# Performance work log

Measured on AMD Instinct MI355X. Metric: run time of the kernel, lower is better.

The kernel has to match this reference:

```python
import jax, jax.numpy as jnp
import numpy as np

EPS = 1e-5
HEADS, K, U, M = 4, 16, 1, 11


def _bn(z, gamma, beta, mean, var):
    # z: [b, c, n]; BN in eval mode (running stats)
    inv = jax.lax.rsqrt(var + EPS)
    return (z - mean[None, :, None]) * (gamma * inv)[None, :, None] + beta[None, :, None]


def setup_inputs() -> dict:
    key = jax.random.key(0)
    ks = jax.random.split(key, 16)
    b, C, w, h = 8, 256, 64, 64
    vv = 256 // HEADS  # out_channels // heads = 64
    inp = {}
    inp['x'] = jax.random.normal(ks[0], (b, C, w, h), dtype=jnp.float32)
    sc = 1.0 / np.sqrt(C)
    inp['Wq'] = jax.random.normal(ks[1], (K * HEADS, C), dtype=jnp.float32) * sc
    inp['q_gamma'] = jnp.ones((K * HEADS,), jnp.float32)
    inp['q_beta'] = jnp.zeros((K * HEADS,), jnp.float32)
    inp['q_mean'] = jax.random.normal(ks[2], (K * HEADS,), dtype=jnp.float32) * 0.1
    inp['q_var'] = jax.random.uniform(ks[3], (K * HEADS,), minval=0.5, maxval=1.5, dtype=jnp.float32)
    inp['Wk'] = jax.random.normal(ks[4], (K * U, C), dtype=jnp.float32) * sc
    inp['Wv'] = jax.random.normal(ks[5], (vv * U, C), dtype=jnp.float32) * sc
    inp['v_gamma'] = jnp.ones((vv * U,), jnp.float32)
    inp['v_beta'] = jnp.zeros((vv * U,), jnp.float32)
    inp['v_mean'] = jax.random.normal(ks[6], (vv * U,), dtype=jnp.float32) * 0.1
    inp['v_var'] = jax.random.uniform(ks[7], (vv * U,), minval=0.5, maxval=1.5, dtype=jnp.float32)
    inp['embedding'] = jax.random.normal(ks[8], (K, U, 1, M, M), dtype=jnp.float32)
    return inp


def reference(x, Wq, q_gamma, q_beta, q_mean, q_var, Wk, Wv,
              v_gamma, v_beta, v_mean, v_var, embedding):
    b, C, w, h = x.shape
    n = w * h
    vv = Wv.shape[0] // U
    xf = x.reshape(b, C, n)

    # queries: 1x1 conv + BN -> [b, heads, k, n]
    q = _bn(jnp.einsum('oc,bcn->bon', Wq, xf), q_gamma, q_beta, q_mean, q_var)
    q = q.reshape(b, HEADS, K, n)

    # keys: 1x1 conv, softmax over spatial positions -> [b, k, u, n]
    keys = jnp.einsum('oc,bcn->bon', Wk, xf).reshape(b, K, U, n)
    sm = jax.nn.softmax(keys, axis=-1)

    # values: 1x1 conv + BN -> [b, vv, u, n]
    values = _bn(jnp.einsum('oc,bcn->bon', Wv, xf), v_gamma, v_beta, v_mean, v_var)
    values = values.reshape(b, vv, U, n)

    # content lambda
    lam_c = jnp.einsum('bkun,bvun->bkv', sm, values)          # [b, k, vv]
    y_c = jnp.einsum('bhkn,bkv->bhvn', q, lam_c)              # [b, h, vv, n]

    # position lambda via conv3d over (vv, w, h) with kernel (1, m, m)
    v5 = values.reshape(b, U, vv, w, h)                       # torch .view reinterpret
    pad = (M - 1) // 2
    lam_p = jax.lax.conv_general_dilated(
        v5, embedding, window_strides=(1, 1, 1),
        padding=((0, 0), (pad, pad), (pad, pad)),
        dimension_numbers=('NCDHW', 'OIDHW', 'NCDHW'))        # [b, k, vv, w, h]
    lam_p = lam_p.reshape(b, K, vv, n)
    y_p = jnp.einsum('bhkn,bkvn->bhvn', q, lam_p)             # [b, h, vv, n]

    out = (y_c + y_p).reshape(b, HEADS * vv, w, h)
    return out
```

## Files before the change

kernel.cpp:

```cpp
#include <hip/hip_runtime.h>
#include <math.h>

#define EPSBN 1e-5f

constexpr int B_ = 8, C_ = 256, N_ = 4096, IMG_ = 64;
constexpr int HEADS_ = 4, K_ = 16, VV_ = 64, M_ = 11, OC_ = 144;

typedef _Float16 half4 __attribute__((ext_vector_type(4)));
typedef _Float16 half8 __attribute__((ext_vector_type(8)));
typedef __fp16 fp16x2 __attribute__((ext_vector_type(2)));
typedef float f32x4 __attribute__((ext_vector_type(4)));

constexpr size_t O_WT   = 0;
constexpr size_t O_BIAS = 18432;
constexpr size_t O_EMBT = 18688;
constexpr size_t O_Q    = 24832;
constexpr size_t O_KEYS = O_Q    + 1048576;
constexpr size_t O_SINV = O_KEYS + 524288;
constexpr size_t O_VP   = 1597952;
constexpr size_t O_LCP  = O_VP   + 1802240;
constexpr size_t O_LC   = O_LCP  + 262144;

constexpr int VPROW = 88, VPPLANE = 80 * 88;

__global__ void k_prep(const float* __restrict__ Wq,
                       const float* __restrict__ qg, const float* __restrict__ qb,
                       const float* __restrict__ qm, const float* __restrict__ qv,
                       const float* __restrict__ Wk, const float* __restrict__ Wv,
                       const float* __restrict__ vg, const float* __restrict__ vb,
                       const float* __restrict__ vm, const float* __restrict__ vva,
                       const float* __restrict__ emb, float* __restrict__ ws) {
    int t = threadIdx.x, blk = blockIdx.x;
    if (blk >= 16) {
        size_t i = (size_t)(blk - 16) * 256 + t;
        f32x4 z = {0.f, 0.f, 0.f, 0.f};
        *(f32x4*)(ws + O_VP + i * 4) = z;
        return;
    }
    _Float16* wf = (_Float16*)(ws + O_WT);
    int base = blk * 2304;
#pragma unroll
    for (int i = 0; i < 9; i++) {
        int idx = base + i * 256 + t;
        int o = idx >> 8, c = idx & 255;
        float w;
        if (o < 64) {
            float s = qg[o] * rsqrtf(qv[o] + EPSBN);
            w = Wq[o * 256 + c] * s;
        } else if (o < 80) {
            w = Wk[(o - 64) * 256 + c];
        } else {
            int ov = o - 80;
            float s = vg[ov] * rsqrtf(vva[ov] + EPSBN);
            w = Wv[ov * 256 + c] * s;
        }
        wf[idx] = (_Float16)w;
    }
    if (blk == 0 && t < 144) {
        float bias;
        if (t < 64) {
            float s = qg[t] * rsqrtf(qv[t] + EPSBN);
            bias = qb[t] - qm[t] * s;
        } else if (t < 80) {
            bias = 0.f;
        } else {
            int ov = t - 80;
            float s = vg[ov] * rsqrtf(vva[ov] + EPSBN);
            bias = vb[ov] - vm[ov] * s;
        }
        ws[O_BIAS + t] = bias;
    }
    if (blk == 15) {
        _Float16* ef = (_Float16*)(ws + O_EMBT);
        for (int idx = t; idx < 64 * 48; idx += 256) {
            int l = idx / 48, rem = idx % 48;
            int dp = rem >> 3, j = rem & 7;
            int k = l & 15, g = l >> 4;
            int dy = 2 * dp + (j >> 2);
            int dx = 4 * g + (j & 3);
            float v = (dy < 11 && dx < 11) ? emb[k * 121 + dy * 11 + dx] : 0.f;
            ef[idx] = (_Float16)v;
        }
    }
}

__global__ __launch_bounds__(256) void k_proj(const float* __restrict__ x,
                                              const float* __restrict__ wsc,
                                              float* __restrict__ ws) {
    __shared__ uint WL[144 * 68];
    __shared__ uint XL[64 * 68];
    int b    = blockIdx.y;
    int pos0 = blockIdx.x * 64;
    int t    = threadIdx.x;
    int w = t >> 6, l = t & 63;
    int g = l >> 4, r = l & 15;

    f32x4 acc[9];
#pragma unroll
    for (int mf = 0; mf < 9; mf++) acc[mf] = (f32x4){0.f, 0.f, 0.f, 0.f};

    const uint* wsrc = (const uint*)(wsc + O_WT);
    const float* xb = x + (size_t)b * C_ * N_ + pos0;
    union u4h { uint4 u; half8 h; };

    for (int kh = 0; kh < 2; kh++) {
        if (kh) __syncthreads();
#pragma unroll
        for (int i = 0; i < 9; i++) {
            int idx = t + i * 256;
            int o = idx >> 4, c4 = idx & 15;
            uint4 wv = *(const uint4*)(wsrc + o * 128 + kh * 64 + c4 * 4);
            *(uint4*)&WL[o * 68 + c4 * 4] = wv;
        }
#pragma unroll
        for (int i = 0; i < 4; i++) {
            int idx = t + i * 256;
            int cl = idx >> 4, p4 = idx & 15;
            float4 a0 = *(const float4*)(xb + (size_t)(2 * (64 * kh + cl)) * N_ + 4 * p4);
            float4 a1 = *(const float4*)(xb + (size_t)(2 * (64 * kh + cl) + 1) * N_ + 4 * p4);
            union { _Float16 h[2]; uint u; } pk;
#pragma unroll
            for (int j = 0; j < 4; j++) {
                float v0 = (j == 0) ? a0.x : (j == 1) ? a0.y : (j == 2) ? a0.z : a0.w;
                float v1 = (j == 0) ? a1.x : (j == 1) ? a1.y : (j == 2) ? a1.z : a1.w;
                pk.h[0] = (_Float16)v0; pk.h[1] = (_Float16)v1;
                XL[(4 * p4 + j) * 68 + cl] = pk.u;
            }
        }
        __syncthreads();

#pragma unroll
        for (int ks = 0; ks < 4; ks++) {
            int cu = 16 * ks + 4 * g;
            u4h bf;
            bf.u = *(const uint4*)&XL[(w * 16 + r) * 68 + cu];
#pragma unroll
            for (int mf = 0; mf < 9; mf++) {
                u4h af;
                af.u = *(const uint4*)&WL[(16 * mf + r) * 68 + cu];
                acc[mf] = __builtin_amdgcn_mfma_f32_16x16x32_f16(af.h, bf.h, acc[mf], 0, 0, 0);
            }
        }
    }

    int pos = pos0 + w * 16 + r;
#pragma unroll
    for (int mf = 0; mf < 9; mf++) {
        float4 bias4 = *(const float4*)(wsc + O_BIAS + 16 * mf + 4 * g);
        f32x4 a = acc[mf];
        float rv0 = a[0] + bias4.x, rv1 = a[1] + bias4.y;
        float rv2 = a[2] + bias4.z, rv3 = a[3] + bias4.w;
        if (mf < 4) {
            union { fp16x2 h[2]; uint2 u; } pk;
            pk.h[0] = __builtin_amdgcn_cvt_pkrtz(rv0, rv1);
            pk.h[1] = __builtin_amdgcn_cvt_pkrtz(rv2, rv3);
            ((uint2*)(ws + O_Q))[((size_t)(b * 16 + 4 * mf + g)) * N_ + pos] = pk.u;
        } else if (mf == 4) {
            int ch0 = 16 * mf + 4 * g;
            float* kp = ws + O_KEYS + ((size_t)(b * 16 + (ch0 - 64))) * N_ + pos;
            kp[0] = rv0; kp[(size_t)N_] = rv1; kp[2 * (size_t)N_] = rv2; kp[3 * (size_t)N_] = rv3;
        } else {
            int ov = 16 * mf + 4 * g - 80;
            int y = pos >> 6, xx = pos & 63;
            _Float16* vp = (_Float16*)(ws + O_VP) +
                           ((size_t)(b * 64 + ov)) * VPPLANE + (size_t)(y + 8) * VPROW + (xx + 8);
            vp[0] = (_Float16)rv0; vp[VPPLANE] = (_Float16)rv1;
            vp[2 * VPPLANE] = (_Float16)rv2; vp[3 * VPPLANE] = (_Float16)rv3;
        }
    }
}

__global__ __launch_bounds__(256) void k_ssum(float* __restrict__ ws) {
    int row = blockIdx.x;
    const float* src = ws + O_KEYS + (size_t)row * N_;
    int t = threadIdx.x;
    float s = 0.f;
#pragma unroll
    for (int i = 0; i < 4; i++) {
        float4 r = *(const float4*)(src + i * 1024 + t * 4);
        s += expf(r.x) + expf(r.y) + expf(r.z) + expf(r.w);
    }
    for (int off = 32; off > 0; off >>= 1) s += __shfl_xor(s, off);
    __shared__ float reds[4];
    if ((t & 63) == 0) reds[t >> 6] = s;
    __syncthreads();
    if (t == 0)
        ws[O_SINV + row] = 1.f / (reds[0] + reds[1] + reds[2] + reds[3]);
}

__global__ __launch_bounds__(256) void k_lamc(float* __restrict__ ws) {
    int b  = blockIdx.x >> 5;
    int ch = blockIdx.x & 31;
    int n0 = ch * 128;
    int y0r = n0 >> 6;
    __shared__ float ek[16 * 128];
    int t = threadIdx.x;
#pragma unroll
    for (int i = 0; i < 2; i++) {
        int f4 = t + i * 256;
        int k = f4 >> 5, nq = f4 & 31;
        float4 kv = *(const float4*)(ws + O_KEYS + ((size_t)(b * 16 + k)) * N_ + n0 + 4 * nq);
        float is = ws[O_SINV + b * 16 + k];
        float4 e;
        e.x = expf(kv.x) * is; e.y = expf(kv.y) * is;
        e.z = expf(kv.z) * is; e.w = expf(kv.w) * is;
        *(float4*)&ek[k * 128 + 4 * nq] = e;
    }
    __syncthreads();

    int v  = t & 63;
    int kg = __builtin_amdgcn_readfirstlane(t >> 6);
    float acc[4] = {0.f, 0.f, 0.f, 0.f};
    const _Float16* vp = (const _Float16*)(ws + O_VP) +
                         (size_t)(b * 64 + v) * VPPLANE + (size_t)(y0r + 8) * VPROW + 8;
#pragma unroll
    for (int r = 0; r < 2; r++) {
        union U4 { uint4 q; _Float16 h[8]; } u[8];
#pragma unroll
        for (int iu = 0; iu < 8; iu++)
            u[iu].q = *(const uint4*)(vp + (size_t)r * VPROW + 8 * iu);
#pragma unroll
        for (int xq = 0; xq < 16; xq++) {
            float4 e0 = *(const float4*)&ek[(kg * 4 + 0) * 128 + r * 64 + 4 * xq];
            float4 e1 = *(const float4*)&ek[(kg * 4 + 1) * 128 + r * 64 + 4 * xq];
            float4 e2 = *(const float4*)&ek[(kg * 4 + 2) * 128 + r * 64 + 4 * xq];
            float4 e3 = *(const float4*)&ek[(kg * 4 + 3) * 128 + r * 64 + 4 * xq];
            float v0 = (float)u[xq >> 1].h[(xq & 1) * 4 + 0];
            float v1 = (float)u[xq >> 1].h[(xq & 1) * 4 + 1];
            float v2 = (float)u[xq >> 1].h[(xq & 1) * 4 + 2];
            float v3 = (float)u[xq >> 1].h[(xq & 1) * 4 + 3];
            acc[0] += e0.x * v0 + e0.y * v1 + e0.z * v2 + e0.w * v3;
            acc[1] += e1.x * v0 + e1.y * v1 + e1.z * v2 + e1.w * v3;
            acc[2] += e2.x * v0 + e2.y * v1 + e2.z * v2 + e2.w * v3;
            acc[3] += e3.x * v0 + e3.y * v1 + e3.z * v2 + e3.w * v3;
        }
    }
#pragma unroll
    for (int j = 0; j < 4; j++)
        ws[O_LCP + ((size_t)(b * 32 + ch) * 16 + kg * 4 + j) * 64 + v] = acc[j];
}

__global__ void k_lcred(float* __restrict__ ws) {
    int b = blockIdx.x, t = threadIdx.x;
    float s = 0.f;
    for (int c = 0; c < 32; c++)
        s += ws[O_LCP + ((size_t)(b * 32 + c)) * 1024 + t];
    ws[O_LC + (size_t)b * 1024 + t] = s;
}

__global__ __launch_bounds__(256, 4) void k_out(const float* __restrict__ wsc,
                                                float* __restrict__ out) {
    __shared__ ushort vt[2][4][19][84];
    int ytile = blockIdx.x;
    int vc    = blockIdx.y;
    int b     = blockIdx.z;
    int y0 = ytile * 8, v0 = vc * 4;
    int t = threadIdx.x;
    int w = t >> 6, l = t & 63;
    int g = l >> 4, nb = l & 15;

    float4 lc4[4];
#pragma unroll
    for (int i = 0; i < 4; i++)
        lc4[i] = *(const float4*)(wsc + O_LC + ((size_t)(b * 16 + 4 * g + i)) * 64 + v0);

    union AF { uint4 u; half8 h; } af[6];
    {
        const uint4* ap = (const uint4*)((const _Float16*)(wsc + O_EMBT) + (size_t)l * 48);
#pragma unroll
        for (int dp = 0; dp < 6; dp++) af[dp].u = ap[dp];
    }

    const ushort* vpb = (const ushort*)(wsc + O_VP) + (size_t)(b * 64 + v0) * VPPLANE;
    for (int T = t; T < 1596; T += 256) {
        int v = T / 399, rem = T % 399;
        int r = rem / 21, qd = rem % 21;
        const ushort* src = vpb + (size_t)v * VPPLANE + (size_t)(y0 + 3 + r) * VPROW + 4 * qd;
        uint2 u01 = *(const uint2*)src;
        uint2 u23 = *(const uint2*)(src + 4);
        *(uint2*)&vt[0][v][r][4 * qd] = u01;
        uint lo = (u01.x >> 16) | (u01.y << 16);
        uint hi = (u01.y >> 16) | (u23.x << 16);
        *(uint2*)&vt[1][v][r][4 * qd] = make_uint2(lo, hi);
    }
    __syncthreads();

    const uint* vtu = (const uint*)&vt[0][0][0][0];
    const uint2* qfp = (const uint2*)(wsc + O_Q);

#pragma unroll
    for (int xt = 0; xt < 4; xt++) {
        int X = xt * 16 + nb;
        union QH { uint2 u; fp16x2 h[2]; } qh[2][4];
#pragma unroll
        for (int yy2 = 0; yy2 < 2; yy2++) {
            int pos = (y0 + 2 * w + yy2) * 64 + X;
#pragma unroll
            for (int j = 0; j < 4; j++)
                qh[yy2][j].u = qfp[((size_t)(b * 16 + 4 * (g ^ j) + g)) * N_ + pos];
        }
        int wcol = X + 4 * g + 3;
        int cp   = wcol & 1;
        int j0u  = (wcol - cp) >> 1;

#pragma unroll
        for (int v = 0; v < 4; v++) {
            int bwin = ((cp * 4 + v) * 19 + 2 * w) * 42 + j0u;
            uint2 win[13];
#pragma unroll
            for (int i = 0; i < 13; i++) {
                win[i].x = vtu[bwin + 42 * i];
                win[i].y = vtu[bwin + 42 * i + 1];
            }

#pragma unroll
            for (int yy2 = 0; yy2 < 2; yy2++) {
                f32x4 acc = {0.f, 0.f, 0.f, 0.f};
#pragma unroll
                for (int dp = 0; dp < 6; dp++) {
                    union { uint u[4]; half8 h; } bb;
                    bb.u[0] = win[yy2 + 2 * dp].x;
                    bb.u[1] = win[yy2 + 2 * dp].y;
                    bb.u[2] = win[yy2 + 2 * dp + 1].x;
                    bb.u[3] = win[yy2 + 2 * dp + 1].y;
                    acc = __builtin_amdgcn_mfma_f32_16x16x32_f16(af[dp].h, bb.h, acc, 0, 0, 0);
                }
                float d0 = acc[0] + lc4[0][v];
                float d1 = acc[1] + lc4[1][v];
                float d2 = acc[2] + lc4[2][v];
                float d3 = acc[3] + lc4[3][v];
                fp16x2 dlo = __builtin_amdgcn_cvt_pkrtz(d0, d1);
                fp16x2 dhi = __builtin_amdgcn_cvt_pkrtz(d2, d3);
                float ph[4];
#pragma unroll
                for (int j = 0; j < 4; j++)
                    ph[j] = __builtin_amdgcn_fdot2(qh[yy2][j].h[0], dlo,
                            __builtin_amdgcn_fdot2(qh[yy2][j].h[1], dhi, 0.f, false), false);
                float sa = ph[0] + __shfl_xor(ph[1], 16);
                float sb = ph[2] + __shfl_xor(ph[3], 16);
                float o  = sa + __shfl_xor(sb, 32);
                int pos = (y0 + 2 * w + yy2) * 64 + X;
                out[((size_t)(b * 256 + g * 64 + v0 + v)) * N_ + pos] = o;
            }
        }
    }
}

extern "C" void kernel_launch(void* const* d_in, const int* in_sizes, int n_in,
                              void* d_out, int out_size, void* d_ws, size_t ws_size,
                              hipStream_t stream) {
    const float* x   = (const float*)d_in[0];
    const float* Wq  = (const float*)d_in[1];
    const float* qg  = (const float*)d_in[2];
    const float* qb  = (const float*)d_in[3];
    const float* qm  = (const float*)d_in[4];
    const float* qv  = (const float*)d_in[5];
    const float* Wk  = (const float*)d_in[6];
    const float* Wv  = (const float*)d_in[7];
    const float* vg  = (const float*)d_in[8];
    const float* vb  = (const float*)d_in[9];
    const float* vm  = (const float*)d_in[10];
    const float* vva = (const float*)d_in[11];
    const float* emb = (const float*)d_in[12];
    float* ws  = (float*)d_ws;
    float* out = (float*)d_out;

    k_prep<<<1776, 256, 0, stream>>>(Wq, qg, qb, qm, qv, Wk, Wv, vg, vb, vm, vva, emb, ws);
    k_proj<<<dim3(64, 8), 256, 0, stream>>>(x, ws, ws);
    k_ssum<<<128, 256, 0, stream>>>(ws);
    k_lamc<<<256, 256, 0, stream>>>(ws);
    k_lcred<<<8, 1024, 0, stream>>>(ws);
    k_out<<<dim3(8, 16, 8), 256, 0, stream>>>(ws, out);
}
```

Baseline: 59.31 us.

## Fuse softmax exp and row-sum into projection epilogue, drop ssum kernel

The projection kernel now applies exp to the key logits, stores the exponentials, and reduces per-block row sums that it adds atomically into a zeroed sum buffer. This removes the separate k_ssum launch and its re-read of the keys, and k_lamc no longer recomputes exp. k_lamc is also split into 512 blocks of one image row each, which doubles the partial buffer that k_lcred has to reduce. Computing exp without subtracting the max risks overflow on larger logits, and the atomic adds make the summation order nondeterministic.

```diff
diff --git a/kernel.cpp b/kernel.cpp
--- a/kernel.cpp
+++ b/kernel.cpp
@@ -19,7 +19,7 @@
 constexpr size_t O_SINV = O_KEYS + 524288;
 constexpr size_t O_VP   = 1597952;
 constexpr size_t O_LCP  = O_VP   + 1802240;
-constexpr size_t O_LC   = O_LCP  + 262144;
+constexpr size_t O_LC   = O_LCP  + 524288;
 
 constexpr int VPROW = 88, VPPLANE = 80 * 88;
 
@@ -56,19 +56,22 @@
         }
         wf[idx] = (_Float16)w;
     }
-    if (blk == 0 && t < 144) {
-        float bias;
-        if (t < 64) {
-            float s = qg[t] * rsqrtf(qv[t] + EPSBN);
-            bias = qb[t] - qm[t] * s;
-        } else if (t < 80) {
-            bias = 0.f;
-        } else {
-            int ov = t - 80;
-            float s = vg[ov] * rsqrtf(vva[ov] + EPSBN);
-            bias = vb[ov] - vm[ov] * s;
-        }
-        ws[O_BIAS + t] = bias;
+    if (blk == 0) {
+        if (t < 144) {
+            float bias;
+            if (t < 64) {
+                float s = qg[t] * rsqrtf(qv[t] + EPSBN);
+                bias = qb[t] - qm[t] * s;
+            } else if (t < 80) {
+                bias = 0.f;
+            } else {
+                int ov = t - 80;
+                float s = vg[ov] * rsqrtf(vva[ov] + EPSBN);
+                bias = vb[ov] - vm[ov] * s;
+            }
+            ws[O_BIAS + t] = bias;
+        }
+        if (t < 128) ws[O_SINV + t] = 0.f;
     }
     if (blk == 15) {
         _Float16* ef = (_Float16*)(ws + O_EMBT);
@@ -89,6 +92,7 @@
                                               float* __restrict__ ws) {
     __shared__ uint WL[144 * 68];
     __shared__ uint XL[64 * 68];
+    __shared__ float pred[4][16];
     int b    = blockIdx.y;
     int pos0 = blockIdx.x * 64;
     int t    = threadIdx.x;
@@ -156,9 +160,21 @@
             pk.h[1] = __builtin_amdgcn_cvt_pkrtz(rv2, rv3);
             ((uint2*)(ws + O_Q))[((size_t)(b * 16 + 4 * mf + g)) * N_ + pos] = pk.u;
         } else if (mf == 4) {
-            int ch0 = 16 * mf + 4 * g;
-            float* kp = ws + O_KEYS + ((size_t)(b * 16 + (ch0 - 64))) * N_ + pos;
-            kp[0] = rv0; kp[(size_t)N_] = rv1; kp[2 * (size_t)N_] = rv2; kp[3 * (size_t)N_] = rv3;
+            int k0 = 4 * g;
+            float e0 = expf(rv0), e1 = expf(rv1), e2 = expf(rv2), e3 = expf(rv3);
+            float* kp = ws + O_KEYS + ((size_t)(b * 16 + k0)) * N_ + pos;
+            kp[0] = e0; kp[(size_t)N_] = e1;
+            kp[2 * (size_t)N_] = e2; kp[3 * (size_t)N_] = e3;
+            float s0 = e0, s1 = e1, s2 = e2, s3 = e3;
+#pragma unroll
+            for (int off = 1; off < 16; off <<= 1) {
+                s0 += __shfl_xor(s0, off); s1 += __shfl_xor(s1, off);
+                s2 += __shfl_xor(s2, off); s3 += __shfl_xor(s3, off);
+            }
+            if (r == 0) {
+                pred[w][k0 + 0] = s0; pred[w][k0 + 1] = s1;
+                pred[w][k0 + 2] = s2; pred[w][k0 + 3] = s3;
+            }
         } else {
             int ov = 16 * mf + 4 * g - 80;
             int y = pos >> 6, xx = pos & 63;
@@ -168,43 +184,26 @@
             vp[2 * VPPLANE] = (_Float16)rv2; vp[3 * VPPLANE] = (_Float16)rv3;
         }
     }
-}
-
-__global__ __launch_bounds__(256) void k_ssum(float* __restrict__ ws) {
-    int row = blockIdx.x;
-    const float* src = ws + O_KEYS + (size_t)row * N_;
+    __syncthreads();
+    if (t < 16) {
+        float s = pred[0][t] + pred[1][t] + pred[2][t] + pred[3][t];
+        atomicAdd(ws + O_SINV + b * 16 + t, s);
+    }
+}
+
+__global__ __launch_bounds__(256) void k_lamc(float* __restrict__ ws) {
+    int b  = blockIdx.x >> 6;
+    int ch = blockIdx.x & 63;
+    int n0 = ch * 64;
+    __shared__ float ek[16 * 64];
     int t = threadIdx.x;
-    float s = 0.f;
-#pragma unroll
-    for (int i = 0; i < 4; i++) {
-        float4 r = *(const float4*)(src + i * 1024 + t * 4);
-        s += expf(r.x) + expf(r.y) + expf(r.z) + expf(r.w);
-    }
-    for (int off = 32; off > 0; off >>= 1) s += __shfl_xor(s, off);
-    __shared__ float reds[4];
-    if ((t & 63) == 0) reds[t >> 6] = s;
-    __syncthreads();
-    if (t == 0)
-        ws[O_SINV + row] = 1.f / (reds[0] + reds[1] + reds[2] + reds[3]);
-}
-
-__global__ __launch_bounds__(256) void k_lamc(float* __restrict__ ws) {
-    int b  = blockIdx.x >> 5;
-    int ch = blockIdx.x & 31;
-    int n0 = ch * 128;
-    int y0r = n0 >> 6;
-    __shared__ float ek[16 * 128];
-    int t = threadIdx.x;
-#pragma unroll
-    for (int i = 0; i < 2; i++) {
-        int f4 = t + i * 256;
-        int k = f4 >> 5, nq = f4 & 31;
+    {
+        int k = t >> 4, nq = t & 15;
         float4 kv = *(const float4*)(ws + O_KEYS + ((size_t)(b * 16 + k)) * N_ + n0 + 4 * nq);
-        float is = ws[O_SINV + b * 16 + k];
+        float is = 1.f / ws[O_SINV + b * 16 + k];
         float4 e;
-        e.x = expf(kv.x) * is; e.y = expf(kv.y) * is;
-        e.z = expf(kv.z) * is; e.w = expf(kv.w) * is;
-        *(float4*)&ek[k * 128 + 4 * nq] = e;
+        e.x = kv.x * is; e.y = kv.y * is; e.z = kv.z * is; e.w = kv.w * is;
+        *(float4*)&ek[k * 64 + 4 * nq] = e;
     }
     __syncthreads();
 
@@ -212,39 +211,36 @@
     int kg = __builtin_amdgcn_readfirstlane(t >> 6);
     float acc[4] = {0.f, 0.f, 0.f, 0.f};
     const _Float16* vp = (const _Float16*)(ws + O_VP) +
-                         (size_t)(b * 64 + v) * VPPLANE + (size_t)(y0r + 8) * VPROW + 8;
-#pragma unroll
-    for (int r = 0; r < 2; r++) {
-        union U4 { uint4 q; _Float16 h[8]; } u[8];
-#pragma unroll
-        for (int iu = 0; iu < 8; iu++)
-            u[iu].q = *(const uint4*)(vp + (size_t)r * VPROW + 8 * iu);
-#pragma unroll
-        for (int xq = 0; xq < 16; xq++) {
-            float4 e0 = *(const float4*)&ek[(kg * 4 + 0) * 128 + r * 64 + 4 * xq];
-            float4 e1 = *(const float4*)&ek[(kg * 4 + 1) * 128 + r * 64 + 4 * xq];
-            float4 e2 = *(const float4*)&ek[(kg * 4 + 2) * 128 + r * 64 + 4 * xq];
-            float4 e3 = *(const float4*)&ek[(kg * 4 + 3) * 128 + r * 64 + 4 * xq];
-            float v0 = (float)u[xq >> 1].h[(xq & 1) * 4 + 0];
-            float v1 = (float)u[xq >> 1].h[(xq & 1) * 4 + 1];
-            float v2 = (float)u[xq >> 1].h[(xq & 1) * 4 + 2];
-            float v3 = (float)u[xq >> 1].h[(xq & 1) * 4 + 3];
-            acc[0] += e0.x * v0 + e0.y * v1 + e0.z * v2 + e0.w * v3;
-            acc[1] += e1.x * v0 + e1.y * v1 + e1.z * v2 + e1.w * v3;
-            acc[2] += e2.x * v0 + e2.y * v1 + e2.z * v2 + e2.w * v3;
-            acc[3] += e3.x * v0 + e3.y * v1 + e3.z * v2 + e3.w * v3;
-        }
+                         (size_t)(b * 64 + v) * VPPLANE + (size_t)(ch + 8) * VPROW + 8;
+    union U4 { uint4 q; _Float16 h[8]; } u[8];
+#pragma unroll
+    for (int iu = 0; iu < 8; iu++)
+        u[iu].q = *(const uint4*)(vp + 8 * iu);
+#pragma unroll
+    for (int xq = 0; xq < 16; xq++) {
+        float4 e0 = *(const float4*)&ek[(kg * 4 + 0) * 64 + 4 * xq];
+        float4 e1 = *(const float4*)&ek[(kg * 4 + 1) * 64 + 4 * xq];
+        float4 e2 = *(const float4*)&ek[(kg * 4 + 2) * 64 + 4 * xq];
+        float4 e3 = *(const float4*)&ek[(kg * 4 + 3) * 64 + 4 * xq];
+        float v0 = (float)u[xq >> 1].h[(xq & 1) * 4 + 0];
+        float v1 = (float)u[xq >> 1].h[(xq & 1) * 4 + 1];
+        float v2 = (float)u[xq >> 1].h[(xq & 1) * 4 + 2];
+        float v3 = (float)u[xq >> 1].h[(xq & 1) * 4 + 3];
+        acc[0] += e0.x * v0 + e0.y * v1 + e0.z * v2 + e0.w * v3;
+        acc[1] += e1.x * v0 + e1.y * v1 + e1.z * v2 + e1.w * v3;
+        acc[2] += e2.x * v0 + e2.y * v1 + e2.z * v2 + e2.w * v3;
+        acc[3] += e3.x * v0 + e3.y * v1 + e3.z * v2 + e3.w * v3;
     }
 #pragma unroll
     for (int j = 0; j < 4; j++)
-        ws[O_LCP + ((size_t)(b * 32 + ch) * 16 + kg * 4 + j) * 64 + v] = acc[j];
+        ws[O_LCP + ((size_t)(b * 64 + ch) * 16 + kg * 4 + j) * 64 + v] = acc[j];
 }
 
 __global__ void k_lcred(float* __restrict__ ws) {
     int b = blockIdx.x, t = threadIdx.x;
     float s = 0.f;
-    for (int c = 0; c < 32; c++)
-        s += ws[O_LCP + ((size_t)(b * 32 + c)) * 1024 + t];
+    for (int c = 0; c < 64; c++)
+        s += ws[O_LCP + ((size_t)(b * 64 + c)) * 1024 + t];
     ws[O_LC + (size_t)b * 1024 + t] = s;
 }
 
@@ -367,8 +363,7 @@
 
     k_prep<<<1776, 256, 0, stream>>>(Wq, qg, qb, qm, qv, Wk, Wv, vg, vb, vm, vva, emb, ws);
     k_proj<<<dim3(64, 8), 256, 0, stream>>>(x, ws, ws);
-    k_ssum<<<128, 256, 0, stream>>>(ws);
-    k_lamc<<<256, 256, 0, stream>>>(ws);
+    k_lamc<<<512, 256, 0, stream>>>(ws);
     k_lcred<<<8, 1024, 0, stream>>>(ws);
     k_out<<<dim3(8, 16, 8), 256, 0, stream>>>(ws, out);
 }
```

New measurement: 60.93 us. 2.7% more time.
